# Kernel tuning notes

Hardware: AMD Instinct MI355X
Metric: run time of the kernel (lower is better)

Reference implementation:

```python
import jax, jax.numpy as jnp
import numpy as np

B, T, N, M, D = 4, 2, 2048, 2048, 3

def _pairwise_sq(a, b):
    # a: [B,N,D], b: [B,M,D] -> squared euclidean distances [B,N,M]
    a2 = jnp.sum(a * a, axis=-1)
    b2 = jnp.sum(b * b, axis=-1)
    ab = jnp.einsum('bnd,bmd->bnm', a, b)
    return jnp.maximum(a2[:, :, None] + b2[:, None, :] - 2.0 * ab, 0.0)


def setup_inputs() -> dict:
    key = jax.random.key(0)
    k1, k2, k3, k4 = jax.random.split(key, 4)
    x = jax.random.uniform(k1, (B, T, N, D), dtype=jnp.float32)
    # m_hat is the frozen motion model's output; small motions keep chamfer mask active
    m_hat = jax.random.uniform(k2, (B, 1, N, D), dtype=jnp.float32) * 0.02
    y_hat0 = jax.random.uniform(k3, (B, 1, M, D), dtype=jnp.float32)
    y_hat1 = jax.random.uniform(k4, (B, 1, M, D), dtype=jnp.float32)
    return {'x': x, 'm_hat': m_hat, 'y_hat0': y_hat0, 'y_hat1': y_hat1}


def reference(x, m_hat, y_hat0, y_hat1):
    sg = jax.lax.stop_gradient
    x_t0 = x[:, 0, :, :3]              # [B,N,3]
    x_t1 = x[:, 1, :, :3]              # [B,N,3]
    x_t1_hat = x_t0 + m_hat[:, 0]      # [B,N,3]

    # chamfer(x_t1_hat, x_t1): squared NN distances both ways
    d = _pairwise_sq(x_t1_hat, x_t1)   # [B,N,N]
    dist1 = jnp.min(d, axis=-1)
    dist2 = jnp.min(d, axis=-2)
    loss_chamfer = dist1.mean(axis=-1) + dist2.mean(axis=-1)          # [B]
    mask_chamfer = sg((loss_chamfer < 0.1).astype(x.dtype))[:, None, None, None]

    y0 = y_hat0[:, 0]                  # [B,M,3]
    dists = jnp.sqrt(_pairwise_sq(y0, x_t0))                          # [B,M,N]
    x_cat = jnp.concatenate([x_t0, x_t1], axis=1)                     # [B,2N,3]
    dists2 = jnp.sqrt(_pairwise_sq(y0, x_cat))                        # [B,M,2N]

    min_dists = jnp.min(dists, axis=-1)        # [B,M]
    min_indices = jnp.argmin(dists, axis=-1)   # [B,M]
    min_dists2 = jnp.min(dists2, axis=-1)      # [B,M]

    mask_dist = sg((min_dists < 0.05).astype(x.dtype))[:, None, :, None]      # [B,1,M,1]
    mask_dist_neg = sg((min_dists2 > 0.2).astype(x.dtype))[:, None, :, None]  # [B,1,M,1]

    nearest_m = jnp.take_along_axis(m_hat[:, 0], min_indices[:, :, None], axis=1)  # [B,M,3]

    # chamfer(x_t0, y_hat0): only dist1 used, masked mean over entries < 0.1
    c1 = jnp.min(_pairwise_sq(x_t0, y0), axis=-1)                     # [B,N]
    sel = c1 < 0.1
    loss_dist = jnp.sum(jnp.where(sel, c1, 0.0)) / jnp.maximum(jnp.sum(sel.astype(c1.dtype)), 1.0)

    pred = (y_hat1 - y_hat0) * mask_chamfer * mask_dist               # [B,1,M,3]
    tgt = nearest_m[:, None, :, :] * mask_chamfer * mask_dist
    loss_dynamic = jnp.mean((pred - tgt) ** 2)

    my_hat_static = (y_hat1 - y_hat0) * mask_dist_neg
    loss_static = jnp.mean(my_hat_static ** 2)

    return (loss_dynamic, loss_static, loss_dist)
```

## Files before the change

### kernel.cpp

```cpp
#include <hip/hip_runtime.h>
#include <math.h>

#define BATCH 4
#define NPTS  2048
#define NT    256
#define ROWS_PT 4
#define CPB     64
#define COLCHUNKS (NPTS / CPB)
#define ROWHALVES 2

#define F4N        (BATCH * NPTS)
#define OFF_PT0    0
#define OFF_PT1    (F4N * 4)
#define OFF_PT1H   (F4N * 8)
#define OFF_PY0    (F4N * 12)
#define OFF_DIST1  (F4N * 16)
#define OFF_DIST2  (OFF_DIST1 + F4N)
#define OFF_C1     (OFF_DIST1 + 2 * F4N)
#define OFF_RM3    (OFF_DIST1 + 3 * F4N)
#define OFF_RM2    (OFF_DIST1 + 4 * F4N)
#define OFF_MASKC  (OFF_RM2 + 2 * F4N)
#define OFF_ACCUM  (OFF_MASKC + 4)

#define INF_BITS 0x7f800000u

__device__ __forceinline__ float sqnorm3(float x, float y, float z) {
    return __fadd_rn(__fadd_rn(__fmul_rn(x, x), __fmul_rn(y, y)), __fmul_rn(z, z));
}

__global__ __launch_bounds__(NT) void prep_kernel(
    const float* __restrict__ x, const float* __restrict__ m_hat,
    const float* __restrict__ y_hat0, float* __restrict__ ws)
{
    int gid = blockIdx.x * NT + threadIdx.x;
    int b = gid >> 11, n = gid & (NPTS - 1);

    const float* xt0 = x + ((size_t)(b * 2 + 0) * NPTS + n) * 3;
    const float* xt1 = x + ((size_t)(b * 2 + 1) * NPTS + n) * 3;
    const float* mh  = m_hat  + ((size_t)b * NPTS + n) * 3;
    const float* yy  = y_hat0 + ((size_t)b * NPTS + n) * 3;

    float a0 = xt0[0], a1 = xt0[1], a2 = xt0[2];
    float c0 = xt1[0], c1v = xt1[1], c2 = xt1[2];
    float h0 = a0 + mh[0], h1 = a1 + mh[1], h2 = a2 + mh[2];
    float y0 = yy[0], y1 = yy[1], y2 = yy[2];

    float4* P = (float4*)ws;
    P[(OFF_PT0  >> 2) + gid] = make_float4(a0, a1, a2, sqnorm3(a0, a1, a2));
    P[(OFF_PT1  >> 2) + gid] = make_float4(c0, c1v, c2, sqnorm3(c0, c1v, c2));
    P[(OFF_PT1H >> 2) + gid] = make_float4(h0, h1, h2, sqnorm3(h0, h1, h2));
    P[(OFF_PY0  >> 2) + gid] = make_float4(y0, y1, y2, sqnorm3(y0, y1, y2));

    unsigned* u = (unsigned*)ws;
    u[OFF_DIST1 + gid] = INF_BITS;
    u[OFF_DIST2 + gid] = INF_BITS;
    u[OFF_C1    + gid] = INF_BITS;
    u[OFF_RM3   + gid] = INF_BITS;
    ((unsigned long long*)(ws + OFF_RM2))[gid] = 0xFFFFFFFFFFFFFFFFull;

    if (gid < 4) ws[OFF_ACCUM + gid] = 0.0f;
}

__global__ __launch_bounds__(NT) void pairwise_kernel(float* __restrict__ ws)
{
    __shared__ float4 tile[CPB];

    int tid = threadIdx.x;
    int rowHalf  = blockIdx.x >> 5;
    int colChunk = blockIdx.x & 31;
    int b    = blockIdx.y;
    int prob = blockIdx.z;

    const float4* P = (const float4*)ws;
    const float4* rows;
    const float4* cols;
    float* out = nullptr;

    switch (prob) {
        case 0: rows = P + (OFF_PT1H >> 2); cols = P + (OFF_PT1  >> 2); out = ws + OFF_DIST1; break;
        case 1: rows = P + (OFF_PT1  >> 2); cols = P + (OFF_PT1H >> 2); out = ws + OFF_DIST2; break;
        case 2: rows = P + (OFF_PY0  >> 2); cols = P + (OFF_PT0  >> 2); break;
        case 3: rows = P + (OFF_PY0  >> 2); cols = P + (OFF_PT1  >> 2); out = ws + OFF_RM3;   break;
        default: rows = P + (OFF_PT0 >> 2); cols = P + (OFF_PY0  >> 2); out = ws + OFF_C1;    break;
    }

    int colBase = colChunk * CPB;
    if (tid < CPB) tile[tid] = cols[(size_t)b * NPTS + colBase + tid];

    int r0 = rowHalf * (NT * ROWS_PT) + tid;
    float4 a[ROWS_PT];
    #pragma unroll
    for (int k = 0; k < ROWS_PT; ++k)
        a[k] = rows[(size_t)b * NPTS + r0 + k * NT];

    __syncthreads();

    if (prob == 2) {
        float best[ROWS_PT];
        int bestIdx[ROWS_PT];
        #pragma unroll
        for (int k = 0; k < ROWS_PT; ++k) { best[k] = __uint_as_float(INF_BITS); bestIdx[k] = 0; }
        #pragma unroll 4
        for (int c = 0; c < CPB; ++c) {
            float4 q = tile[c];
            #pragma unroll
            for (int k = 0; k < ROWS_PT; ++k) {
                float dot = a[k].x * q.x + a[k].y * q.y + a[k].z * q.z;
                float d = __fsub_rn(__fadd_rn(a[k].w, q.w), __fmul_rn(2.0f, dot));
                d = fmaxf(d, 0.0f);
                if (d < best[k]) { best[k] = d; bestIdx[k] = c; }
            }
        }
        #pragma unroll
        for (int k = 0; k < ROWS_PT; ++k) {
            unsigned long long key =
                ((unsigned long long)__float_as_uint(best[k]) << 32) |
                (unsigned)(colBase + bestIdx[k]);
            atomicMin(((unsigned long long*)(ws + OFF_RM2)) + (size_t)b * NPTS + r0 + k * NT, key);
        }
    } else {
        float best[ROWS_PT];
        #pragma unroll
        for (int k = 0; k < ROWS_PT; ++k) best[k] = __uint_as_float(INF_BITS);
        #pragma unroll 4
        for (int c = 0; c < CPB; ++c) {
            float4 q = tile[c];
            #pragma unroll
            for (int k = 0; k < ROWS_PT; ++k) {
                float dot = a[k].x * q.x + a[k].y * q.y + a[k].z * q.z;
                float d = __fsub_rn(__fadd_rn(a[k].w, q.w), __fmul_rn(2.0f, dot));
                d = fmaxf(d, 0.0f);
                best[k] = fminf(best[k], d);
            }
        }
        #pragma unroll
        for (int k = 0; k < ROWS_PT; ++k)
            atomicMin((unsigned*)(out + (size_t)b * NPTS + r0 + k * NT), __float_as_uint(best[k]));
    }
}

__global__ __launch_bounds__(NT) void reduce_kernel(float* __restrict__ ws)
{
    int b = blockIdx.x, tid = threadIdx.x;
    const float* dist1 = ws + OFF_DIST1 + (size_t)b * NPTS;
    const float* dist2 = ws + OFF_DIST2 + (size_t)b * NPTS;
    const float* c1    = ws + OFF_C1    + (size_t)b * NPTS;

    float s1 = 0.f, s2 = 0.f, cs = 0.f, cc = 0.f;
    for (int i = tid; i < NPTS; i += NT) {
        s1 += dist1[i];
        s2 += dist2[i];
        float c = c1[i];
        if (c < 0.1f) { cs += c; cc += 1.0f; }
    }
    #pragma unroll
    for (int off = 32; off > 0; off >>= 1) {
        s1 += __shfl_down(s1, off);
        s2 += __shfl_down(s2, off);
        cs += __shfl_down(cs, off);
        cc += __shfl_down(cc, off);
    }
    __shared__ float sm[4][4];
    int wv = tid >> 6, ln = tid & 63;
    if (ln == 0) { sm[wv][0] = s1; sm[wv][1] = s2; sm[wv][2] = cs; sm[wv][3] = cc; }
    __syncthreads();
    if (tid == 0) {
        float t1 = sm[0][0] + sm[1][0] + sm[2][0] + sm[3][0];
        float t2 = sm[0][1] + sm[1][1] + sm[2][1] + sm[3][1];
        float tc = sm[0][2] + sm[1][2] + sm[2][2] + sm[3][2];
        float tn = sm[0][3] + sm[1][3] + sm[2][3] + sm[3][3];
        float loss_chamfer = t1 / (float)NPTS + t2 / (float)NPTS;
        ws[OFF_MASKC + b] = (loss_chamfer < 0.1f) ? 1.0f : 0.0f;
        atomicAdd(ws + OFF_ACCUM + 0, tc);
        atomicAdd(ws + OFF_ACCUM + 1, tn);
    }
}

__global__ __launch_bounds__(NT) void finalize_kernel(
    const float* __restrict__ m_hat, const float* __restrict__ y_hat0,
    const float* __restrict__ y_hat1, float* __restrict__ ws)
{
    int gid = blockIdx.x * NT + threadIdx.x;
    int b = gid >> 11;

    unsigned long long key = ((const unsigned long long*)(ws + OFF_RM2))[gid];
    float d2 = __uint_as_float((unsigned)(key >> 32));
    unsigned idx = (unsigned)(key & 0xFFFFFFFFull);
    float rm3 = ws[OFF_RM3 + gid];

    float md   = (sqrtf(d2) < 0.05f) ? 1.0f : 0.0f;
    float dcat = fminf(d2, rm3);
    float mneg = (sqrtf(dcat) > 0.2f) ? 1.0f : 0.0f;
    float w = ws[OFF_MASKC + b] * md;

    const float* p0 = y_hat0 + (size_t)gid * 3;
    const float* p1 = y_hat1 + (size_t)gid * 3;
    const float* nm = m_hat + ((size_t)b * NPTS + idx) * 3;

    float dyn = 0.f, stat = 0.f;
    #pragma unroll
    for (int k = 0; k < 3; ++k) {
        float diff = p1[k] - p0[k];
        float e = w * (diff - nm[k]);
        dyn += e * e;
        float s = mneg * diff;
        stat += s * s;
    }
    #pragma unroll
    for (int off = 32; off > 0; off >>= 1) {
        dyn  += __shfl_down(dyn, off);
        stat += __shfl_down(stat, off);
    }
    __shared__ float sd[4], ss[4];
    int wv = threadIdx.x >> 6, ln = threadIdx.x & 63;
    if (ln == 0) { sd[wv] = dyn; ss[wv] = stat; }
    __syncthreads();
    if (threadIdx.x == 0) {
        atomicAdd(ws + OFF_ACCUM + 2, sd[0] + sd[1] + sd[2] + sd[3]);
        atomicAdd(ws + OFF_ACCUM + 3, ss[0] + ss[1] + ss[2] + ss[3]);
    }
}

__global__ void writeout_kernel(const float* __restrict__ ws, float* __restrict__ out)
{
    const float denom = (float)(BATCH * NPTS * 3);
    out[0] = ws[OFF_ACCUM + 2] / denom;
    out[1] = ws[OFF_ACCUM + 3] / denom;
    out[2] = ws[OFF_ACCUM + 0] / fmaxf(ws[OFF_ACCUM + 1], 1.0f);
}

extern "C" void kernel_launch(void* const* d_in, const int* in_sizes, int n_in,
                              void* d_out, int out_size, void* d_ws, size_t ws_size,
                              hipStream_t stream)
{
    const float* x      = (const float*)d_in[0];
    const float* m_hat  = (const float*)d_in[1];
    const float* y_hat0 = (const float*)d_in[2];
    const float* y_hat1 = (const float*)d_in[3];
    float* ws  = (float*)d_ws;
    float* out = (float*)d_out;

    prep_kernel<<<dim3((BATCH * NPTS) / NT), dim3(NT), 0, stream>>>(x, m_hat, y_hat0, ws);
    pairwise_kernel<<<dim3(ROWHALVES * COLCHUNKS, BATCH, 5), dim3(NT), 0, stream>>>(ws);
    reduce_kernel<<<dim3(BATCH), dim3(NT), 0, stream>>>(ws);
    finalize_kernel<<<dim3((BATCH * NPTS) / NT), dim3(NT), 0, stream>>>(m_hat, y_hat0, y_hat1, ws);
    writeout_kernel<<<dim3(1), dim3(1), 0, stream>>>(ws, out);
}
```

Baseline: 86.48 us.

## Replace atomics with per-chunk partial minima and fuse prep/reduce into fewer kernels

Removes the prep kernel by computing points and squared norms inline while loading tiles. Pairwise blocks now write per-column-chunk partial minima to workspace instead of using atomicMin. A new row-reduce kernel merges those partials and fuses the chamfer, mask and loss reductions, and a single final kernel applies the per-batch chamfer mask. The launch count drops from five to three and atomics disappear. In exchange the partial arrays add extra workspace traffic, and the point conversion is recomputed in every block.

```diff
diff --git a/kernel.cpp b/kernel.cpp
--- a/kernel.cpp
+++ b/kernel.cpp
@@ -8,60 +8,59 @@
 #define CPB     64
 #define COLCHUNKS (NPTS / CPB)
 #define ROWHALVES 2
-
-#define F4N        (BATCH * NPTS)
-#define OFF_PT0    0
-#define OFF_PT1    (F4N * 4)
-#define OFF_PT1H   (F4N * 8)
-#define OFF_PY0    (F4N * 12)
-#define OFF_DIST1  (F4N * 16)
-#define OFF_DIST2  (OFF_DIST1 + F4N)
-#define OFF_C1     (OFF_DIST1 + 2 * F4N)
-#define OFF_RM3    (OFF_DIST1 + 3 * F4N)
-#define OFF_RM2    (OFF_DIST1 + 4 * F4N)
-#define OFF_MASKC  (OFF_RM2 + 2 * F4N)
-#define OFF_ACCUM  (OFF_MASKC + 4)
+#define ROWS_TOT  (BATCH * NPTS)
+
+#define OFF_PD1   0
+#define OFF_PD2   (COLCHUNKS * ROWS_TOT)
+#define OFF_PC1   (2 * COLCHUNKS * ROWS_TOT)
+#define OFF_PRM3  (3 * COLCHUNKS * ROWS_TOT)
+#define OFF_PRM2  (4 * COLCHUNKS * ROWS_TOT)
+#define OFF_BLK   (6 * COLCHUNKS * ROWS_TOT)
 
 #define INF_BITS 0x7f800000u
+
+typedef unsigned long long ull;
 
 __device__ __forceinline__ float sqnorm3(float x, float y, float z) {
     return __fadd_rn(__fadd_rn(__fmul_rn(x, x), __fmul_rn(y, y)), __fmul_rn(z, z));
 }
 
-__global__ __launch_bounds__(NT) void prep_kernel(
+#define SRC_T0  0
+#define SRC_T1  1
+#define SRC_T1H 2
+#define SRC_Y0  3
+
+__device__ __forceinline__ float4 make_point(int src, int b, int i,
+    const float* __restrict__ x, const float* __restrict__ m_hat,
+    const float* __restrict__ y_hat0)
+{
+    float px, py, pz;
+    if (src == SRC_Y0) {
+        const float* p = y_hat0 + ((size_t)b * NPTS + i) * 3;
+        px = p[0]; py = p[1]; pz = p[2];
+    } else if (src == SRC_T1) {
+        const float* p = x + ((size_t)(b * 2 + 1) * NPTS + i) * 3;
+        px = p[0]; py = p[1]; pz = p[2];
+    } else {
+        const float* p = x + ((size_t)(b * 2 + 0) * NPTS + i) * 3;
+        px = p[0]; py = p[1]; pz = p[2];
+        if (src == SRC_T1H) {
+            const float* mh = m_hat + ((size_t)b * NPTS + i) * 3;
+            px += mh[0]; py += mh[1]; pz += mh[2];
+        }
+    }
+    return make_float4(px, py, pz, sqnorm3(px, py, pz));
+}
+
+__device__ __forceinline__ ull shfl_xor_u64(ull v, int m) {
+    int lo = __shfl_xor((int)(v & 0xFFFFFFFFull), m);
+    int hi = __shfl_xor((int)(v >> 32), m);
+    return ((ull)(unsigned)hi << 32) | (unsigned)lo;
+}
+
+__global__ __launch_bounds__(NT) void pairwise_kernel(
     const float* __restrict__ x, const float* __restrict__ m_hat,
     const float* __restrict__ y_hat0, float* __restrict__ ws)
-{
-    int gid = blockIdx.x * NT + threadIdx.x;
-    int b = gid >> 11, n = gid & (NPTS - 1);
-
-    const float* xt0 = x + ((size_t)(b * 2 + 0) * NPTS + n) * 3;
-    const float* xt1 = x + ((size_t)(b * 2 + 1) * NPTS + n) * 3;
-    const float* mh  = m_hat  + ((size_t)b * NPTS + n) * 3;
-    const float* yy  = y_hat0 + ((size_t)b * NPTS + n) * 3;
-
-    float a0 = xt0[0], a1 = xt0[1], a2 = xt0[2];
-    float c0 = xt1[0], c1v = xt1[1], c2 = xt1[2];
-    float h0 = a0 + mh[0], h1 = a1 + mh[1], h2 = a2 + mh[2];
-    float y0 = yy[0], y1 = yy[1], y2 = yy[2];
-
-    float4* P = (float4*)ws;
-    P[(OFF_PT0  >> 2) + gid] = make_float4(a0, a1, a2, sqnorm3(a0, a1, a2));
-    P[(OFF_PT1  >> 2) + gid] = make_float4(c0, c1v, c2, sqnorm3(c0, c1v, c2));
-    P[(OFF_PT1H >> 2) + gid] = make_float4(h0, h1, h2, sqnorm3(h0, h1, h2));
-    P[(OFF_PY0  >> 2) + gid] = make_float4(y0, y1, y2, sqnorm3(y0, y1, y2));
-
-    unsigned* u = (unsigned*)ws;
-    u[OFF_DIST1 + gid] = INF_BITS;
-    u[OFF_DIST2 + gid] = INF_BITS;
-    u[OFF_C1    + gid] = INF_BITS;
-    u[OFF_RM3   + gid] = INF_BITS;
-    ((unsigned long long*)(ws + OFF_RM2))[gid] = 0xFFFFFFFFFFFFFFFFull;
-
-    if (gid < 4) ws[OFF_ACCUM + gid] = 0.0f;
-}
-
-__global__ __launch_bounds__(NT) void pairwise_kernel(float* __restrict__ ws)
 {
     __shared__ float4 tile[CPB];
 
@@ -71,27 +70,23 @@
     int b    = blockIdx.y;
     int prob = blockIdx.z;
 
-    const float4* P = (const float4*)ws;
-    const float4* rows;
-    const float4* cols;
-    float* out = nullptr;
-
+    int rsrc, csrc, outOff;
     switch (prob) {
-        case 0: rows = P + (OFF_PT1H >> 2); cols = P + (OFF_PT1  >> 2); out = ws + OFF_DIST1; break;
-        case 1: rows = P + (OFF_PT1  >> 2); cols = P + (OFF_PT1H >> 2); out = ws + OFF_DIST2; break;
-        case 2: rows = P + (OFF_PY0  >> 2); cols = P + (OFF_PT0  >> 2); break;
-        case 3: rows = P + (OFF_PY0  >> 2); cols = P + (OFF_PT1  >> 2); out = ws + OFF_RM3;   break;
-        default: rows = P + (OFF_PT0 >> 2); cols = P + (OFF_PY0  >> 2); out = ws + OFF_C1;    break;
+        case 0:  rsrc = SRC_T1H; csrc = SRC_T1;  outOff = OFF_PD1;  break;
+        case 1:  rsrc = SRC_T1;  csrc = SRC_T1H; outOff = OFF_PD2;  break;
+        case 2:  rsrc = SRC_Y0;  csrc = SRC_T0;  outOff = -1;       break;
+        case 3:  rsrc = SRC_Y0;  csrc = SRC_T1;  outOff = OFF_PRM3; break;
+        default: rsrc = SRC_T0;  csrc = SRC_Y0;  outOff = OFF_PC1;  break;
     }
 
     int colBase = colChunk * CPB;
-    if (tid < CPB) tile[tid] = cols[(size_t)b * NPTS + colBase + tid];
+    if (tid < CPB) tile[tid] = make_point(csrc, b, colBase + tid, x, m_hat, y_hat0);
 
     int r0 = rowHalf * (NT * ROWS_PT) + tid;
     float4 a[ROWS_PT];
     #pragma unroll
     for (int k = 0; k < ROWS_PT; ++k)
-        a[k] = rows[(size_t)b * NPTS + r0 + k * NT];
+        a[k] = make_point(rsrc, b, r0 + k * NT, x, m_hat, y_hat0);
 
     __syncthreads();
 
@@ -111,12 +106,12 @@
                 if (d < best[k]) { best[k] = d; bestIdx[k] = c; }
             }
         }
+        ull* prm2 = (ull*)(ws + OFF_PRM2);
         #pragma unroll
         for (int k = 0; k < ROWS_PT; ++k) {
-            unsigned long long key =
-                ((unsigned long long)__float_as_uint(best[k]) << 32) |
-                (unsigned)(colBase + bestIdx[k]);
-            atomicMin(((unsigned long long*)(ws + OFF_RM2)) + (size_t)b * NPTS + r0 + k * NT, key);
+            ull key = ((ull)__float_as_uint(best[k]) << 32) |
+                      (unsigned)(colBase + bestIdx[k]);
+            prm2[(size_t)colChunk * ROWS_TOT + b * NPTS + r0 + k * NT] = key;
         }
     } else {
         float best[ROWS_PT];
@@ -135,98 +130,121 @@
         }
         #pragma unroll
         for (int k = 0; k < ROWS_PT; ++k)
-            atomicMin((unsigned*)(out + (size_t)b * NPTS + r0 + k * NT), __float_as_uint(best[k]));
-    }
-}
-
-__global__ __launch_bounds__(NT) void reduce_kernel(float* __restrict__ ws)
-{
-    int b = blockIdx.x, tid = threadIdx.x;
-    const float* dist1 = ws + OFF_DIST1 + (size_t)b * NPTS;
-    const float* dist2 = ws + OFF_DIST2 + (size_t)b * NPTS;
-    const float* c1    = ws + OFF_C1    + (size_t)b * NPTS;
-
-    float s1 = 0.f, s2 = 0.f, cs = 0.f, cc = 0.f;
-    for (int i = tid; i < NPTS; i += NT) {
-        s1 += dist1[i];
-        s2 += dist2[i];
-        float c = c1[i];
-        if (c < 0.1f) { cs += c; cc += 1.0f; }
-    }
-    #pragma unroll
-    for (int off = 32; off > 0; off >>= 1) {
-        s1 += __shfl_down(s1, off);
-        s2 += __shfl_down(s2, off);
-        cs += __shfl_down(cs, off);
-        cc += __shfl_down(cc, off);
-    }
-    __shared__ float sm[4][4];
-    int wv = tid >> 6, ln = tid & 63;
-    if (ln == 0) { sm[wv][0] = s1; sm[wv][1] = s2; sm[wv][2] = cs; sm[wv][3] = cc; }
-    __syncthreads();
-    if (tid == 0) {
-        float t1 = sm[0][0] + sm[1][0] + sm[2][0] + sm[3][0];
-        float t2 = sm[0][1] + sm[1][1] + sm[2][1] + sm[3][1];
-        float tc = sm[0][2] + sm[1][2] + sm[2][2] + sm[3][2];
-        float tn = sm[0][3] + sm[1][3] + sm[2][3] + sm[3][3];
-        float loss_chamfer = t1 / (float)NPTS + t2 / (float)NPTS;
-        ws[OFF_MASKC + b] = (loss_chamfer < 0.1f) ? 1.0f : 0.0f;
-        atomicAdd(ws + OFF_ACCUM + 0, tc);
-        atomicAdd(ws + OFF_ACCUM + 1, tn);
-    }
-}
-
-__global__ __launch_bounds__(NT) void finalize_kernel(
+            ws[outOff + (size_t)colChunk * ROWS_TOT + b * NPTS + r0 + k * NT] = best[k];
+    }
+}
+
+__global__ __launch_bounds__(NT) void rowreduce_kernel(
     const float* __restrict__ m_hat, const float* __restrict__ y_hat0,
     const float* __restrict__ y_hat1, float* __restrict__ ws)
 {
-    int gid = blockIdx.x * NT + threadIdx.x;
-    int b = gid >> 11;
-
-    unsigned long long key = ((const unsigned long long*)(ws + OFF_RM2))[gid];
-    float d2 = __uint_as_float((unsigned)(key >> 32));
-    unsigned idx = (unsigned)(key & 0xFFFFFFFFull);
-    float rm3 = ws[OFF_RM3 + gid];
-
-    float md   = (sqrtf(d2) < 0.05f) ? 1.0f : 0.0f;
-    float dcat = fminf(d2, rm3);
+    int tid  = threadIdx.x;
+    int row  = blockIdx.x * 128 + (tid >> 1);
+    int half = tid & 1;
+    int b    = row >> 11;
+
+    const ull* prm2 = (const ull*)(ws + OFF_PRM2);
+
+    float d1m = __uint_as_float(INF_BITS), d2m = d1m, c1m = d1m, r3m = d1m;
+    ull k2 = ~0ull;
+    #pragma unroll
+    for (int c = 0; c < 16; ++c) {
+        int idx = (half * 16 + c) * ROWS_TOT + row;
+        d1m = fminf(d1m, ws[OFF_PD1 + idx]);
+        d2m = fminf(d2m, ws[OFF_PD2 + idx]);
+        c1m = fminf(c1m, ws[OFF_PC1 + idx]);
+        r3m = fminf(r3m, ws[OFF_PRM3 + idx]);
+        ull kk = prm2[idx];
+        k2 = (kk < k2) ? kk : k2;
+    }
+    d1m = fminf(d1m, __shfl_xor(d1m, 1));
+    d2m = fminf(d2m, __shfl_xor(d2m, 1));
+    c1m = fminf(c1m, __shfl_xor(c1m, 1));
+    r3m = fminf(r3m, __shfl_xor(r3m, 1));
+    { ull o = shfl_xor_u64(k2, 1); k2 = (o < k2) ? o : k2; }
+
+    float d2sq = __uint_as_float((unsigned)(k2 >> 32));
+    unsigned idxm = (unsigned)(k2 & 0xFFFFFFFFull);
+    float md   = (sqrtf(d2sq) < 0.05f) ? 1.0f : 0.0f;
+    float dcat = fminf(d2sq, r3m);
     float mneg = (sqrtf(dcat) > 0.2f) ? 1.0f : 0.0f;
-    float w = ws[OFF_MASKC + b] * md;
-
-    const float* p0 = y_hat0 + (size_t)gid * 3;
-    const float* p1 = y_hat1 + (size_t)gid * 3;
-    const float* nm = m_hat + ((size_t)b * NPTS + idx) * 3;
+
+    const float* p0 = y_hat0 + (size_t)row * 3;
+    const float* p1 = y_hat1 + (size_t)row * 3;
+    const float* nm = m_hat + ((size_t)b * NPTS + idxm) * 3;
 
     float dyn = 0.f, stat = 0.f;
     #pragma unroll
     for (int k = 0; k < 3; ++k) {
         float diff = p1[k] - p0[k];
-        float e = w * (diff - nm[k]);
+        float e = md * (diff - nm[k]);
         dyn += e * e;
         float s = mneg * diff;
         stat += s * s;
     }
+    float cs = (c1m < 0.1f) ? c1m : 0.f;
+    float cn = (c1m < 0.1f) ? 1.f  : 0.f;
+    float s1 = d1m, s2 = d2m;
+    if (half) { s1 = s2 = cs = cn = dyn = stat = 0.f; }
+
     #pragma unroll
     for (int off = 32; off > 0; off >>= 1) {
-        dyn  += __shfl_down(dyn, off);
-        stat += __shfl_down(stat, off);
-    }
-    __shared__ float sd[4], ss[4];
-    int wv = threadIdx.x >> 6, ln = threadIdx.x & 63;
-    if (ln == 0) { sd[wv] = dyn; ss[wv] = stat; }
+        s1  += __shfl_down(s1,  off);
+        s2  += __shfl_down(s2,  off);
+        cs  += __shfl_down(cs,  off);
+        cn  += __shfl_down(cn,  off);
+        dyn += __shfl_down(dyn, off);
+        stat+= __shfl_down(stat,off);
+    }
+    __shared__ float sm[4][6];
+    int wv = tid >> 6, ln = tid & 63;
+    if (ln == 0) {
+        sm[wv][0] = s1; sm[wv][1] = s2; sm[wv][2] = cs;
+        sm[wv][3] = cn; sm[wv][4] = dyn; sm[wv][5] = stat;
+    }
     __syncthreads();
-    if (threadIdx.x == 0) {
-        atomicAdd(ws + OFF_ACCUM + 2, sd[0] + sd[1] + sd[2] + sd[3]);
-        atomicAdd(ws + OFF_ACCUM + 3, ss[0] + ss[1] + ss[2] + ss[3]);
-    }
-}
-
-__global__ void writeout_kernel(const float* __restrict__ ws, float* __restrict__ out)
-{
-    const float denom = (float)(BATCH * NPTS * 3);
-    out[0] = ws[OFF_ACCUM + 2] / denom;
-    out[1] = ws[OFF_ACCUM + 3] / denom;
-    out[2] = ws[OFF_ACCUM + 0] / fmaxf(ws[OFF_ACCUM + 1], 1.0f);
+    if (tid == 0) {
+        #pragma unroll
+        for (int j = 0; j < 6; ++j)
+            ws[OFF_BLK + blockIdx.x * 8 + j] = sm[0][j] + sm[1][j] + sm[2][j] + sm[3][j];
+    }
+}
+
+__global__ void final_kernel(const float* __restrict__ ws, float* __restrict__ out)
+{
+    int lane = threadIdx.x;
+    float v[6];
+    #pragma unroll
+    for (int j = 0; j < 6; ++j) v[j] = ws[OFF_BLK + lane * 8 + j];
+    #pragma unroll
+    for (int off = 8; off > 0; off >>= 1) {
+        #pragma unroll
+        for (int j = 0; j < 6; ++j) {
+            float t = __shfl_down(v[j], off);
+            if (((lane & 15) + off) < 16) v[j] += t;
+        }
+    }
+    __shared__ float bs[4][6];
+    if ((lane & 15) == 0) {
+        #pragma unroll
+        for (int j = 0; j < 6; ++j) bs[lane >> 4][j] = v[j];
+    }
+    __syncthreads();
+    if (lane == 0) {
+        float dyn = 0.f, stat = 0.f, cs = 0.f, cn = 0.f;
+        for (int b = 0; b < 4; ++b) {
+            float lc = bs[b][0] / (float)NPTS + bs[b][1] / (float)NPTS;
+            float maskc = (lc < 0.1f) ? 1.0f : 0.0f;
+            dyn  += maskc * bs[b][4];
+            stat += bs[b][5];
+            cs   += bs[b][2];
+            cn   += bs[b][3];
+        }
+        const float denom = (float)(BATCH * NPTS * 3);
+        out[0] = dyn / denom;
+        out[1] = stat / denom;
+        out[2] = cs / fmaxf(cn, 1.0f);
+    }
 }
 
 extern "C" void kernel_launch(void* const* d_in, const int* in_sizes, int n_in,
@@ -240,9 +258,9 @@
     float* ws  = (float*)d_ws;
     float* out = (float*)d_out;
 
-    prep_kernel<<<dim3((BATCH * NPTS) / NT), dim3(NT), 0, stream>>>(x, m_hat, y_hat0, ws);
-    pairwise_kernel<<<dim3(ROWHALVES * COLCHUNKS, BATCH, 5), dim3(NT), 0, stream>>>(ws);
-    reduce_kernel<<<dim3(BATCH), dim3(NT), 0, stream>>>(ws);
-    finalize_kernel<<<dim3((BATCH * NPTS) / NT), dim3(NT), 0, stream>>>(m_hat, y_hat0, y_hat1, ws);
-    writeout_kernel<<<dim3(1), dim3(1), 0, stream>>>(ws, out);
-}
+    pairwise_kernel<<<dim3(ROWHALVES * COLCHUNKS, BATCH, 5), dim3(NT), 0, stream>>>(
+        x, m_hat, y_hat0, ws);
+    rowreduce_kernel<<<dim3(ROWS_TOT / 128), dim3(NT), 0, stream>>>(
+        m_hat, y_hat0, y_hat1, ws);
+    final_kernel<<<dim3(1), dim3(64), 0, stream>>>(ws, out);
+}
```

Result: no change. 86.43 us (-0.1%).
